# Performance work log

Measured on AMD Instinct MI355X. Metric: run time of the kernel, lower is better.

## Reference

```python
import jax, jax.numpy as jnp
import numpy as np
from jax import lax

# Dimensions (see shape_source)
B, J, I, E, H = 256, 128, 64, 512, 512   # batch, target len, source len, embed, hidden
MAXJW = 128                               # max jump width
WJ = 2 * MAXJW + 1                        # size of jump-width set (257)
ALPHA_P0 = 1.0
EPS = 1e-29


def setup_inputs() -> dict:
    key = jax.random.key(0)
    ks = jax.random.split(key, 10)
    return {
        "y_hidden": jax.random.normal(ks[0], (B, J, E), jnp.float32),
        "y_hidden_null": jax.random.normal(ks[1], (1, 1, E), jnp.float32),
        "W_trans": jax.random.normal(ks[2], (E, H), jnp.float32) * 0.02,
        "b_trans": jnp.zeros((H,), jnp.float32),
        "W_jump": jax.random.normal(ks[3], (H, WJ), jnp.float32) * 0.02,
        "b_jump": jnp.zeros((WJ,), jnp.float32),
        "W_p0": jax.random.normal(ks[4], (H, 1), jnp.float32) * 0.02,
        "b_p0": jnp.zeros((1,), jnp.float32),
        # emission probs p(source_t | target_state_k), kept near 1 to avoid
        # underflow of the unrescaled HMM forward product (as in original).
        "emission": jax.random.uniform(ks[5], (B, 2 * J, I), jnp.float32) * 0.5 + 0.75,
        "source_lengths": jax.random.randint(ks[6], (B,), 1, I + 1, dtype=jnp.int32),
        "target_lengths": jax.random.randint(ks[7], (B,), 1, J + 1, dtype=jnp.int32),
    }


def _build_transition(y_hidden, y_hidden_null, W_trans, b_trans, W_jump, b_jump, W_p0, b_p0):
    # get_transition: Dense(tanh) -> Dense(softmax) jump widths; Dense(sigmoid) p0.
    ts = jnp.tanh(y_hidden @ W_trans + b_trans)           # [B,J,H]
    ts_null = jnp.tanh(y_hidden_null @ W_trans + b_trans) # [1,1,H]
    jump_prob = jax.nn.softmax(ts @ W_jump + b_jump, axis=-1)  # [B,J,WJ]
    p0_scalar = ALPHA_P0 * jax.nn.sigmoid(ts_null @ W_p0 + b_p0)[0, 0, 0]
    p0 = jnp.broadcast_to(p0_scalar, (y_hidden.shape[0], J))  # tile to [B,J]
    # gather jump widths: row i takes jump_prob[:, i, MAXJW + k - i] for k in [0,J)
    idx = MAXJW + jnp.arange(J)[None, :] - jnp.arange(J)[:, None]        # [J,J]
    idxb = jnp.broadcast_to(idx[None], (jump_prob.shape[0], J, J))
    jw = jnp.take_along_axis(jump_prob, idxb, axis=2)                    # [B,J,J]
    jw = jw * (1.0 - p0[:, :, None]) / jnp.sum(jw, axis=2, keepdims=True)
    diag_p0 = p0[:, :, None] * jnp.eye(J, dtype=jw.dtype)                # [B,J,J]
    T_half = jnp.concatenate([jw, diag_p0], axis=2)                      # [B,J,2J]
    return jnp.concatenate([T_half, T_half], axis=1)                     # [B,2J,2J]


def reference(y_hidden, y_hidden_null, W_trans, b_trans, W_jump, b_jump,
              W_p0, b_p0, emission, source_lengths, target_lengths):
    T = _build_transition(y_hidden, y_hidden_null, W_trans, b_trans,
                          W_jump, b_jump, W_p0, b_p0)       # [B,2J,2J]
    e = jnp.transpose(emission, (2, 0, 1))                  # [I,B,2J]
    # tf.scan with no initializer: f_0 = emission at source position 0
    f0 = e[0]

    def step(f, et):
        f_next = jnp.einsum('bj,bjk->bk', f, T) * et        # forward recursion
        return f_next, f_next

    _, fs = lax.scan(step, f0, e[1:])
    fs = jnp.concatenate([f0[None], fs], axis=0)            # [I,B,2J]
    fbt = jnp.transpose(fs, (1, 2, 0))                      # [B,2J,I]
    last_idx = (source_lengths - 1).astype(jnp.int32)[:, None, None]
    last = jnp.take_along_axis(fbt, last_idx, axis=2)[:, :, 0]  # [B,2J]
    m = (jnp.arange(J)[None, :] < target_lengths[:, None]).astype(last.dtype)
    mask = jnp.concatenate([m, m], axis=1)                  # [B,2J]
    return jnp.log(jnp.sum(last * mask, axis=1) + EPS)      # [B]
```

## Files before the change

kernel.cpp:

```cpp
#include <hip/hip_runtime.h>
#include <stdint.h>

typedef __attribute__((ext_vector_type(8))) short bf16x8;
typedef __attribute__((ext_vector_type(4))) float f32x4;

__device__ __forceinline__ unsigned short f2bf(float f) {
  union { float f; unsigned int u; } un; un.f = f;
  unsigned int r = un.u + 0x7fffu + ((un.u >> 16) & 1u);
  return (unsigned short)(r >> 16);
}

__device__ __forceinline__ float bf2f(unsigned short u) {
  union { unsigned int u; float f; } un; un.u = ((unsigned int)u) << 16;
  return un.f;
}

__device__ __forceinline__ float tanh_fast(float x) {
  x = fminf(15.f, fmaxf(-15.f, x));
  float e = __expf(2.f * x);
  return (e - 1.f) / (e + 1.f);
}

__device__ __forceinline__ unsigned int cvt_pk_bf16(float lo, float hi) {
  unsigned int r;
  asm("v_cvt_pk_bf16_f32 %0, %1, %2" : "=v"(r) : "v"(lo), "v"(hi));
  return r;
}

__device__ __forceinline__ void gload_lds16(const void* g, void* l) {
  __builtin_amdgcn_global_load_lds(
      (const __attribute__((address_space(1))) unsigned int*)(unsigned long long)g,
      (__attribute__((address_space(3))) unsigned int*)(unsigned int)(unsigned long long)l,
      16, 0, 0);
}

__global__ __launch_bounds__(256) void cvt_weights(
    const float* __restrict__ Wt_in, const float* __restrict__ Wj_in,
    unsigned short* __restrict__ wt, unsigned short* __restrict__ wj) {
  const int i = blockIdx.x * 256 + threadIdx.x;
  if (i < 512 * 512) {
    const int c = i >> 9, r = i & 511;
    wt[i] = f2bf(Wt_in[(size_t)r * 512 + c]);
  } else {
    const int j = i - 512 * 512;
    const int c = j >> 9, r = j & 511;
    wj[j] = f2bf(Wj_in[(size_t)r * 257 + c]);
  }
}

__global__ __launch_bounds__(512) void p0_kernel(
    const float* __restrict__ ynull, const float* __restrict__ W_trans,
    const float* __restrict__ b_trans, const float* __restrict__ W_p0,
    const float* __restrict__ b_p0, float* __restrict__ p0buf) {
  __shared__ float red[512];
  const int hh = threadIdx.x;
  float acc = 0.f;
  for (int e = 0; e < 512; ++e) acc = fmaf(ynull[e], W_trans[(size_t)e * 512 + hh], acc);
  const float ts = tanhf(acc + b_trans[hh]);
  red[hh] = ts * W_p0[hh];
  __syncthreads();
  for (int s = 256; s > 0; s >>= 1) {
    if (hh < s) red[hh] += red[hh + s];
    __syncthreads();
  }
  if (hh == 0) {
    const float z = red[0] + b_p0[0];
    const float p0 = 1.f / (1.f + __expf(-z));
    p0buf[0] = p0;
    p0buf[1] = 1.f - p0;
  }
}


__global__ __launch_bounds__(256, 2) void gemm_af32(
    const float* __restrict__ A, const unsigned short* __restrict__ Bt,
    const float* __restrict__ bias, unsigned short* __restrict__ Cout,
    int M, int N, int K) {
  __shared__ unsigned short sA[2][128 * 32];
  __shared__ unsigned short sB[2][128 * 32];
  const int tid = threadIdx.x;
  const int lane = tid & 63;
  const int wave = tid >> 6;
  const int wr = wave >> 1, wc = wave & 1;
  const int m0 = blockIdx.x * 128, n0 = blockIdx.y * 128;

  f32x4 acc[4][4] = {};

  const int srow = lane >> 2;
  const int sl = lane & 3;
  const int scol = sl * 8;
  const int wsz = (srow >> 1) & 3;
  const int scolw = (sl ^ wsz) * 8;
  const int c0 = wave * 2, c1 = wave * 2 + 1;
  const float* Af0 = A + (size_t)(m0 + c0 * 16 + srow) * K + scol;
  const float* Af1 = A + (size_t)(m0 + c1 * 16 + srow) * K + scol;
  const unsigned short* Br0 = Bt + (size_t)(n0 + c0 * 16 + srow) * K + scolw;
  const unsigned short* Br1 = Bt + (size_t)(n0 + c1 * 16 + srow) * K + scolw;

  const int r15 = lane & 15;
  const int oslot = ((lane >> 4) ^ ((r15 >> 1) & 3)) * 8;
  const int nt = K >> 5;

  auto writeA = [&](int bi, const float4& v00, const float4& v01,
                    const float4& v10, const float4& v11) {
    union { unsigned int u[4]; bf16x8 v; } p;
    p.u[0] = cvt_pk_bf16(v00.x, v00.y);
    p.u[1] = cvt_pk_bf16(v00.z, v00.w);
    p.u[2] = cvt_pk_bf16(v01.x, v01.y);
    p.u[3] = cvt_pk_bf16(v01.z, v01.w);
    *reinterpret_cast<bf16x8*>(&sA[bi][c0 * 512 + srow * 32 + scolw]) = p.v;
    p.u[0] = cvt_pk_bf16(v10.x, v10.y);
    p.u[1] = cvt_pk_bf16(v10.z, v10.w);
    p.u[2] = cvt_pk_bf16(v11.x, v11.y);
    p.u[3] = cvt_pk_bf16(v11.z, v11.w);
    *reinterpret_cast<bf16x8*>(&sA[bi][c1 * 512 + srow * 32 + scolw]) = p.v;
  };
  auto stageB = [&](int bi, int t) {
    gload_lds16(Br0 + t * 32, &sB[bi][c0 * 512]);
    gload_lds16(Br1 + t * 32, &sB[bi][c1 * 512]);
  };
  auto compute = [&](int bi) {
    bf16x8 af[4], bfr[4];
#pragma unroll
    for (int mi = 0; mi < 4; ++mi)
      af[mi] = *reinterpret_cast<const bf16x8*>(
          &sA[bi][(wr * 64 + mi * 16 + r15) * 32 + oslot]);
#pragma unroll
    for (int ni = 0; ni < 4; ++ni)
      bfr[ni] = *reinterpret_cast<const bf16x8*>(
          &sB[bi][(wc * 64 + ni * 16 + r15) * 32 + oslot]);
#pragma unroll
    for (int mi = 0; mi < 4; ++mi)
#pragma unroll
      for (int ni = 0; ni < 4; ++ni)
        acc[mi][ni] = __builtin_amdgcn_mfma_f32_16x16x32_bf16(
            af[mi], bfr[ni], acc[mi][ni], 0, 0, 0);
  };

  float4 x0 = *reinterpret_cast<const float4*>(Af0);
  float4 x1 = *reinterpret_cast<const float4*>(Af0 + 4);
  float4 x2 = *reinterpret_cast<const float4*>(Af1);
  float4 x3 = *reinterpret_cast<const float4*>(Af1 + 4);
  float4 y0 = *reinterpret_cast<const float4*>(Af0 + 32);
  float4 y1 = *reinterpret_cast<const float4*>(Af0 + 36);
  float4 y2 = *reinterpret_cast<const float4*>(Af1 + 32);
  float4 y3 = *reinterpret_cast<const float4*>(Af1 + 36);
  writeA(0, x0, x1, x2, x3);
  stageB(0, 0);
  __syncthreads();

  for (int t = 0; t < nt; t += 2) {
    if (t + 1 < nt) {
      writeA(1, y0, y1, y2, y3);
      stageB(1, t + 1);
    }
    if (t + 2 < nt) {
      x0 = *reinterpret_cast<const float4*>(Af0 + (t + 2) * 32);
      x1 = *reinterpret_cast<const float4*>(Af0 + (t + 2) * 32 + 4);
      x2 = *reinterpret_cast<const float4*>(Af1 + (t + 2) * 32);
      x3 = *reinterpret_cast<const float4*>(Af1 + (t + 2) * 32 + 4);
    }
    compute(0);
    __syncthreads();
    if (t + 2 < nt) {
      writeA(0, x0, x1, x2, x3);
      stageB(0, t + 2);
    }
    if (t + 3 < nt) {
      y0 = *reinterpret_cast<const float4*>(Af0 + (t + 3) * 32);
      y1 = *reinterpret_cast<const float4*>(Af0 + (t + 3) * 32 + 4);
      y2 = *reinterpret_cast<const float4*>(Af1 + (t + 3) * 32);
      y3 = *reinterpret_cast<const float4*>(Af1 + (t + 3) * 32 + 4);
    }
    if (t + 1 < nt) compute(1);
    __syncthreads();
  }

  const int crow0 = m0 + wr * 64 + (lane >> 4) * 4;
  const int ccol0 = n0 + wc * 64 + r15;
#pragma unroll
  for (int mi = 0; mi < 4; ++mi) {
#pragma unroll
    for (int ni = 0; ni < 4; ++ni) {
      const int gcol = ccol0 + ni * 16;
      const float bv = bias[gcol];
#pragma unroll
      for (int r = 0; r < 4; ++r) {
        const int grow = crow0 + mi * 16 + r;
        Cout[(size_t)grow * N + gcol] = f2bf(tanh_fast(acc[mi][ni][r] + bv));
      }
    }
  }
}

__global__ __launch_bounds__(256, 2) void gemm_tt(
    const unsigned short* __restrict__ A, const unsigned short* __restrict__ Bt,
    const float* __restrict__ bias, unsigned short* __restrict__ Cout,
    int M, int N, int K) {
  __shared__ unsigned short sA[2][128 * 32];
  __shared__ unsigned short sB[2][128 * 32];
  const int tid = threadIdx.x;
  const int lane = tid & 63;
  const int wave = tid >> 6;
  const int wr = wave >> 1, wc = wave & 1;
  const int m0 = blockIdx.x * 128, n0 = blockIdx.y * 128;

  f32x4 acc[4][4] = {};

  const int srow = lane >> 2;
  const int sl = lane & 3;
  const int wsz = (srow >> 1) & 3;
  const int scolw = (sl ^ wsz) * 8;
  const int c0 = wave * 2, c1 = wave * 2 + 1;
  const unsigned short* Ar0 = A + (size_t)(m0 + c0 * 16 + srow) * K + scolw;
  const unsigned short* Ar1 = A + (size_t)(m0 + c1 * 16 + srow) * K + scolw;
  const unsigned short* Br0 = Bt + (size_t)(n0 + c0 * 16 + srow) * K + scolw;
  const unsigned short* Br1 = Bt + (size_t)(n0 + c1 * 16 + srow) * K + scolw;

  const int r15 = lane & 15;
  const int oslot = ((lane >> 4) ^ ((r15 >> 1) & 3)) * 8;
  const int nt = K >> 5;

  auto stage = [&](int bi, int t) {
    gload_lds16(Ar0 + t * 32, &sA[bi][c0 * 512]);
    gload_lds16(Ar1 + t * 32, &sA[bi][c1 * 512]);
    gload_lds16(Br0 + t * 32, &sB[bi][c0 * 512]);
    gload_lds16(Br1 + t * 32, &sB[bi][c1 * 512]);
  };
  auto compute = [&](int bi) {
    bf16x8 af[4], bfr[4];
#pragma unroll
    for (int mi = 0; mi < 4; ++mi)
      af[mi] = *reinterpret_cast<const bf16x8*>(
          &sA[bi][(wr * 64 + mi * 16 + r15) * 32 + oslot]);
#pragma unroll
    for (int ni = 0; ni < 4; ++ni)
      bfr[ni] = *reinterpret_cast<const bf16x8*>(
          &sB[bi][(wc * 64 + ni * 16 + r15) * 32 + oslot]);
#pragma unroll
    for (int mi = 0; mi < 4; ++mi)
#pragma unroll
      for (int ni = 0; ni < 4; ++ni)
        acc[mi][ni] = __builtin_amdgcn_mfma_f32_16x16x32_bf16(
            af[mi], bfr[ni], acc[mi][ni], 0, 0, 0);
  };

  stage(0, 0);
  __syncthreads();
  for (int t = 0; t < nt; t += 2) {
    if (t + 1 < nt) stage(1, t + 1);
    compute(0);
    __syncthreads();
    if (t + 2 < nt) stage(0, t + 2);
    if (t + 1 < nt) compute(1);
    __syncthreads();
  }

  const int crow0 = m0 + wr * 64 + (lane >> 4) * 4;
  const int ccol0 = n0 + wc * 64 + r15;
#pragma unroll
  for (int mi = 0; mi < 4; ++mi) {
#pragma unroll
    for (int ni = 0; ni < 4; ++ni) {
      const int gcol = ccol0 + ni * 16;
      const float bv = bias[gcol];
#pragma unroll
      for (int r = 0; r < 4; ++r) {
        const int grow = crow0 + mi * 16 + r;
        Cout[(size_t)grow * N + gcol] = f2bf(acc[mi][ni][r] + bv);
      }
    }
  }
}

__global__ __launch_bounds__(256) void wsoftmax_kernel(
    const unsigned short* __restrict__ logits, const float* __restrict__ p0buf,
    unsigned short* __restrict__ jwout) {
  const int lane = threadIdx.x & 63;
  const int wave = threadIdx.x >> 6;
  const int row = blockIdx.x * 4 + wave;
  const int i = row & 127;
  const unsigned short* lrow = logits + (size_t)row * 256 + (128 - i);
  const float v0 = bf2f(lrow[lane]);
  const float v1 = bf2f(lrow[lane + 64]);
  float mx = fmaxf(v0, v1);
#pragma unroll
  for (int off = 32; off > 0; off >>= 1) mx = fmaxf(mx, __shfl_xor(mx, off));
  const float e0 = __expf(v0 - mx);
  const float e1 = __expf(v1 - mx);
  float s = e0 + e1;
#pragma unroll
  for (int off = 32; off > 0; off >>= 1) s += __shfl_xor(s, off);
  const float scale = p0buf[1] / s;
  unsigned short* orow = jwout + (size_t)row * 128;
  orow[lane] = f2bf(e0 * scale);
  orow[lane + 64] = f2bf(e1 * scale);
}

#define SE_STRIDE 264
__global__ __launch_bounds__(256, 1) void forward_fused(
    const unsigned short* __restrict__ jwb,
    const float* __restrict__ emission,
    const float* __restrict__ p0buf, const int* __restrict__ slen_p,
    const int* __restrict__ tlen_p, float* __restrict__ out) {
  __shared__ __align__(16) float se[64 * SE_STRIDE];
  __shared__ __align__(16) unsigned short gl16[128];
  const int b = blockIdx.x;
  const int tid = threadIdx.x;
  const float* eb = emission + (size_t)b * 16384;

  bf16x8 bfr[4][8];
  const int l = tid & 63;
  const int m = l & 15;
  const int q = l >> 4;

  if (tid >= 64) {
#pragma unroll
    for (int it = 0; it < 6; ++it) {
      const int tau = (tid - 64) + 192 * it;
      if (tau < 1024) {
        const int t0 = (tau & 15) * 4;
        const int mm = (tau >> 4) & 15;
        const int nt0 = ((tau >> 8) & 1) * 4;
        const int half = (tau >> 9) & 1;
        const int kbase = half * 128 + nt0 * 16 + mm;
        const float4 v0 = *reinterpret_cast<const float4*>(&eb[(size_t)(kbase) * 64 + t0]);
        const float4 v1 = *reinterpret_cast<const float4*>(&eb[(size_t)(kbase + 16) * 64 + t0]);
        const float4 v2 = *reinterpret_cast<const float4*>(&eb[(size_t)(kbase + 32) * 64 + t0]);
        const float4 v3 = *reinterpret_cast<const float4*>(&eb[(size_t)(kbase + 48) * 64 + t0]);
        const int jinv0 = half * 128 + mm * 8 + nt0;
        float* d = &se[(size_t)t0 * SE_STRIDE + jinv0];
        *reinterpret_cast<float4*>(d) = (float4){v0.x, v1.x, v2.x, v3.x};
        *reinterpret_cast<float4*>(d + SE_STRIDE) = (float4){v0.y, v1.y, v2.y, v3.y};
        *reinterpret_cast<float4*>(d + 2 * SE_STRIDE) = (float4){v0.z, v1.z, v2.z, v3.z};
        *reinterpret_cast<float4*>(d + 3 * SE_STRIDE) = (float4){v0.w, v1.w, v2.w, v3.w};
      }
    }
  } else {
    const unsigned short* jwt = jwb + (size_t)b * 16384;
#pragma unroll
    for (int kt = 0; kt < 4; ++kt) {
      const int r0 = kt * 32 + q * 8;
#pragma unroll
      for (int nt = 0; nt < 8; ++nt) {
        const int c = nt * 16 + m;
        bf16x8 v;
#pragma unroll
        for (int j = 0; j < 8; ++j) v[j] = (short)jwt[(size_t)(r0 + j) * 128 + c];
        bfr[kt][nt] = v;
      }
    }
  }
  __syncthreads();
  if (tid >= 64) return;

  const float p0 = p0buf[0];
  const int S = slen_p[b];
  const int T = tlen_p[b];

  float gown[8];
  {
    const float4 i0a = *reinterpret_cast<const float4*>(&se[m * 8]);
    const float4 i0b = *reinterpret_cast<const float4*>(&se[m * 8 + 4]);
    const float4 i1a = *reinterpret_cast<const float4*>(&se[128 + m * 8]);
    const float4 i1b = *reinterpret_cast<const float4*>(&se[128 + m * 8 + 4]);
    gown[0] = i0a.x + i1a.x; gown[1] = i0a.y + i1a.y;
    gown[2] = i0a.z + i1a.z; gown[3] = i0a.w + i1a.w;
    gown[4] = i0b.x + i1b.x; gown[5] = i0b.y + i1b.y;
    gown[6] = i0b.z + i1b.z; gown[7] = i0b.w + i1b.w;
  }
  gl16[(2 * q) * 16 + m]     = f2bf(gown[2 * q]);
  gl16[(2 * q + 1) * 16 + m] = f2bf(gown[2 * q + 1]);

  for (int t = 1; t < S; ++t) {
    const float* st = &se[(size_t)t * SE_STRIDE];
    const float4 pe0a = *reinterpret_cast<const float4*>(&st[m * 8]);
    const float4 pe0b = *reinterpret_cast<const float4*>(&st[m * 8 + 4]);
    const float4 pe1a = *reinterpret_cast<const float4*>(&st[128 + m * 8]);
    const float4 pe1b = *reinterpret_cast<const float4*>(&st[128 + m * 8 + 4]);
    const float e0[8] = {pe0a.x, pe0a.y, pe0a.z, pe0a.w, pe0b.x, pe0b.y, pe0b.z, pe0b.w};
    const float e1[8] = {pe1a.x, pe1a.y, pe1a.z, pe1a.w, pe1b.x, pe1b.y, pe1b.z, pe1b.w};
    float h[8];
#pragma unroll
    for (int nt = 0; nt < 8; ++nt) h[nt] = gown[nt] * (p0 * e1[nt]);
    bf16x8 af[4];
#pragma unroll
    for (int kt = 0; kt < 4; ++kt)
      af[kt] = *reinterpret_cast<const bf16x8*>(&gl16[kt * 32 + q * 8]);
    f32x4 acc[8];
#pragma unroll
    for (int nt = 0; nt < 8; ++nt) {
      f32x4 a = __builtin_amdgcn_mfma_f32_16x16x32_bf16(
          af[0], bfr[0][nt], (f32x4){0.f, 0.f, 0.f, 0.f}, 0, 0, 0);
      a = __builtin_amdgcn_mfma_f32_16x16x32_bf16(af[1], bfr[1][nt], a, 0, 0, 0);
      a = __builtin_amdgcn_mfma_f32_16x16x32_bf16(af[2], bfr[2][nt], a, 0, 0, 0);
      acc[nt] = __builtin_amdgcn_mfma_f32_16x16x32_bf16(af[3], bfr[3][nt], a, 0, 0, 0);
    }
#pragma unroll
    for (int nt = 0; nt < 8; ++nt) gown[nt] = fmaf(acc[nt][0], e0[nt], h[nt]);
    gl16[(2 * q) * 16 + m]     = f2bf(gown[2 * q]);
    gl16[(2 * q + 1) * 16 + m] = f2bf(gown[2 * q + 1]);
  }

  float val = 0.f;
#pragma unroll
  for (int nt = 0; nt < 8; ++nt)
    if (nt * 16 + m < T) val += gown[nt];
#pragma unroll
  for (int off = 1; off < 16; off <<= 1) val += __shfl_xor(val, off);
  if (l == 0) out[b] = logf(val + 1e-29f);
}

extern "C" void kernel_launch(void* const* d_in, const int* in_sizes, int n_in,
                              void* d_out, int out_size, void* d_ws, size_t ws_size,
                              hipStream_t stream) {
  const float* y_hidden = (const float*)d_in[0];
  const float* y_null   = (const float*)d_in[1];
  const float* W_trans  = (const float*)d_in[2];
  const float* b_trans  = (const float*)d_in[3];
  const float* W_jump   = (const float*)d_in[4];
  const float* b_jump   = (const float*)d_in[5];
  const float* W_p0     = (const float*)d_in[6];
  const float* b_p0     = (const float*)d_in[7];
  const float* emission = (const float*)d_in[8];
  const int* slen = (const int*)d_in[9];
  const int* tlen = (const int*)d_in[10];
  float* out = (float*)d_out;

  char* ws = (char*)d_ws;
  unsigned short* ts16  = (unsigned short*)ws;
  unsigned short* lg16  = (unsigned short*)(ws + 33554432);
  unsigned short* wt16t = (unsigned short*)(ws + 50331648);
  unsigned short* wj16t = (unsigned short*)(ws + 50855936);
  float* p0buf          = (float*)(ws + 51118080);
  unsigned short* jwb16 = (unsigned short*)(ws + 51118336);

  cvt_weights<<<dim3(1536), dim3(256), 0, stream>>>(W_trans, W_jump, wt16t, wj16t);
  p0_kernel<<<dim3(1), dim3(512), 0, stream>>>(y_null, W_trans, b_trans, W_p0, b_p0, p0buf);

  gemm_af32<<<dim3(256, 4), dim3(256), 0, stream>>>(y_hidden, wt16t, b_trans, ts16,
                                                    32768, 512, 512);
  gemm_tt<<<dim3(256, 2), dim3(256), 0, stream>>>(ts16, wj16t, b_jump, lg16,
                                                  32768, 256, 512);
  wsoftmax_kernel<<<dim3(8192), dim3(256), 0, stream>>>(lg16, p0buf, jwb16);
  forward_fused<<<dim3(256), dim3(256), 0, stream>>>(jwb16, emission, p0buf,
                                                     slen, tlen, out);
}
```

Measured before the change: 116.2 us.

## Restructure GEMMs to stage B half-panels in LDS and stream A from registers

Both projection GEMMs are rewritten to load a 128x256 half of the B (weight) panel into LDS at a time with an XOR swizzle. Each wave now owns 32 full rows and reads A fragments directly from global memory into registers, converting fp32 to bf16 inline for the first GEMM. This removes the per-32-K double-buffered LDS staging of A and most of the barriers. In exchange there is no overlap between B staging and compute, A loads are issued per-wave without LDS sharing, and LDS use rises to 64KB per block, which may limit occupancy.

```diff
diff --git a/kernel.cpp b/kernel.cpp
--- a/kernel.cpp
+++ b/kernel.cpp
@@ -72,202 +72,130 @@
 }
 
 
-__global__ __launch_bounds__(256, 2) void gemm_af32(
+__device__ __forceinline__ void stage_half(
+    const unsigned short* __restrict__ Bt, unsigned short* sB,
+    int n0, int h, int wave, int lane) {
+  const int ln = lane >> 5;
+  const int slot = lane & 31;
+#pragma unroll
+  for (int c = 0; c < 16; ++c) {
+    const int cw = wave * 16 + c;
+    const int row = 2 * cw + ln;
+    const unsigned short* src =
+        Bt + (size_t)(n0 + row) * 512 + h * 256 + ((slot ^ (row & 7)) * 8);
+    gload_lds16(src, &sB[cw * 512]);
+  }
+}
+
+__global__ __launch_bounds__(256, 2) void gemm1_panel(
     const float* __restrict__ A, const unsigned short* __restrict__ Bt,
-    const float* __restrict__ bias, unsigned short* __restrict__ Cout,
-    int M, int N, int K) {
-  __shared__ unsigned short sA[2][128 * 32];
-  __shared__ unsigned short sB[2][128 * 32];
+    const float* __restrict__ bias, unsigned short* __restrict__ Cout) {
+  __shared__ unsigned short sB[128 * 256];
   const int tid = threadIdx.x;
   const int lane = tid & 63;
   const int wave = tid >> 6;
-  const int wr = wave >> 1, wc = wave & 1;
+  const int r15 = lane & 15;
+  const int q = lane >> 4;
   const int m0 = blockIdx.x * 128, n0 = blockIdx.y * 128;
 
-  f32x4 acc[4][4] = {};
-
-  const int srow = lane >> 2;
-  const int sl = lane & 3;
-  const int scol = sl * 8;
-  const int wsz = (srow >> 1) & 3;
-  const int scolw = (sl ^ wsz) * 8;
-  const int c0 = wave * 2, c1 = wave * 2 + 1;
-  const float* Af0 = A + (size_t)(m0 + c0 * 16 + srow) * K + scol;
-  const float* Af1 = A + (size_t)(m0 + c1 * 16 + srow) * K + scol;
-  const unsigned short* Br0 = Bt + (size_t)(n0 + c0 * 16 + srow) * K + scolw;
-  const unsigned short* Br1 = Bt + (size_t)(n0 + c1 * 16 + srow) * K + scolw;
-
-  const int r15 = lane & 15;
-  const int oslot = ((lane >> 4) ^ ((r15 >> 1) & 3)) * 8;
-  const int nt = K >> 5;
-
-  auto writeA = [&](int bi, const float4& v00, const float4& v01,
-                    const float4& v10, const float4& v11) {
-    union { unsigned int u[4]; bf16x8 v; } p;
-    p.u[0] = cvt_pk_bf16(v00.x, v00.y);
-    p.u[1] = cvt_pk_bf16(v00.z, v00.w);
-    p.u[2] = cvt_pk_bf16(v01.x, v01.y);
-    p.u[3] = cvt_pk_bf16(v01.z, v01.w);
-    *reinterpret_cast<bf16x8*>(&sA[bi][c0 * 512 + srow * 32 + scolw]) = p.v;
-    p.u[0] = cvt_pk_bf16(v10.x, v10.y);
-    p.u[1] = cvt_pk_bf16(v10.z, v10.w);
-    p.u[2] = cvt_pk_bf16(v11.x, v11.y);
-    p.u[3] = cvt_pk_bf16(v11.z, v11.w);
-    *reinterpret_cast<bf16x8*>(&sA[bi][c1 * 512 + srow * 32 + scolw]) = p.v;
-  };
-  auto stageB = [&](int bi, int t) {
-    gload_lds16(Br0 + t * 32, &sB[bi][c0 * 512]);
-    gload_lds16(Br1 + t * 32, &sB[bi][c1 * 512]);
-  };
-  auto compute = [&](int bi) {
-    bf16x8 af[4], bfr[4];
-#pragma unroll
-    for (int mi = 0; mi < 4; ++mi)
-      af[mi] = *reinterpret_cast<const bf16x8*>(
-          &sA[bi][(wr * 64 + mi * 16 + r15) * 32 + oslot]);
-#pragma unroll
-    for (int ni = 0; ni < 4; ++ni)
-      bfr[ni] = *reinterpret_cast<const bf16x8*>(
-          &sB[bi][(wc * 64 + ni * 16 + r15) * 32 + oslot]);
-#pragma unroll
-    for (int mi = 0; mi < 4; ++mi)
-#pragma unroll
-      for (int ni = 0; ni < 4; ++ni)
-        acc[mi][ni] = __builtin_amdgcn_mfma_f32_16x16x32_bf16(
-            af[mi], bfr[ni], acc[mi][ni], 0, 0, 0);
-  };
-
-  float4 x0 = *reinterpret_cast<const float4*>(Af0);
-  float4 x1 = *reinterpret_cast<const float4*>(Af0 + 4);
-  float4 x2 = *reinterpret_cast<const float4*>(Af1);
-  float4 x3 = *reinterpret_cast<const float4*>(Af1 + 4);
-  float4 y0 = *reinterpret_cast<const float4*>(Af0 + 32);
-  float4 y1 = *reinterpret_cast<const float4*>(Af0 + 36);
-  float4 y2 = *reinterpret_cast<const float4*>(Af1 + 32);
-  float4 y3 = *reinterpret_cast<const float4*>(Af1 + 36);
-  writeA(0, x0, x1, x2, x3);
-  stageB(0, 0);
-  __syncthreads();
-
-  for (int t = 0; t < nt; t += 2) {
-    if (t + 1 < nt) {
-      writeA(1, y0, y1, y2, y3);
-      stageB(1, t + 1);
-    }
-    if (t + 2 < nt) {
-      x0 = *reinterpret_cast<const float4*>(Af0 + (t + 2) * 32);
-      x1 = *reinterpret_cast<const float4*>(Af0 + (t + 2) * 32 + 4);
-      x2 = *reinterpret_cast<const float4*>(Af1 + (t + 2) * 32);
-      x3 = *reinterpret_cast<const float4*>(Af1 + (t + 2) * 32 + 4);
-    }
-    compute(0);
-    __syncthreads();
-    if (t + 2 < nt) {
-      writeA(0, x0, x1, x2, x3);
-      stageB(0, t + 2);
-    }
-    if (t + 3 < nt) {
-      y0 = *reinterpret_cast<const float4*>(Af0 + (t + 3) * 32);
-      y1 = *reinterpret_cast<const float4*>(Af0 + (t + 3) * 32 + 4);
-      y2 = *reinterpret_cast<const float4*>(Af1 + (t + 3) * 32);
-      y3 = *reinterpret_cast<const float4*>(Af1 + (t + 3) * 32 + 4);
-    }
-    if (t + 1 < nt) compute(1);
-    __syncthreads();
-  }
-
-  const int crow0 = m0 + wr * 64 + (lane >> 4) * 4;
-  const int ccol0 = n0 + wc * 64 + r15;
-#pragma unroll
-  for (int mi = 0; mi < 4; ++mi) {
-#pragma unroll
-    for (int ni = 0; ni < 4; ++ni) {
-      const int gcol = ccol0 + ni * 16;
+  f32x4 acc[2][8] = {};
+  const float* Arow0 = A + (size_t)(m0 + wave * 32 + r15) * 512;
+  const float* Arow1 = A + (size_t)(m0 + wave * 32 + 16 + r15) * 512;
+  const int sxor = r15 & 7;
+
+  for (int h = 0; h < 2; ++h) {
+    stage_half(Bt, sB, n0, h, wave, lane);
+    __syncthreads();
+#pragma unroll 2
+    for (int kk = 0; kk < 8; ++kk) {
+      const int col = h * 256 + kk * 32 + q * 8;
+      bf16x8 af[2];
+      {
+        const float4 lo0 = *reinterpret_cast<const float4*>(Arow0 + col);
+        const float4 hi0 = *reinterpret_cast<const float4*>(Arow0 + col + 4);
+        const float4 lo1 = *reinterpret_cast<const float4*>(Arow1 + col);
+        const float4 hi1 = *reinterpret_cast<const float4*>(Arow1 + col + 4);
+        union { unsigned int u[4]; bf16x8 v; } p;
+        p.u[0] = cvt_pk_bf16(lo0.x, lo0.y); p.u[1] = cvt_pk_bf16(lo0.z, lo0.w);
+        p.u[2] = cvt_pk_bf16(hi0.x, hi0.y); p.u[3] = cvt_pk_bf16(hi0.z, hi0.w);
+        af[0] = p.v;
+        p.u[0] = cvt_pk_bf16(lo1.x, lo1.y); p.u[1] = cvt_pk_bf16(lo1.z, lo1.w);
+        p.u[2] = cvt_pk_bf16(hi1.x, hi1.y); p.u[3] = cvt_pk_bf16(hi1.z, hi1.w);
+        af[1] = p.v;
+      }
+      const int s0 = kk * 4 + q;
+#pragma unroll
+      for (int ni = 0; ni < 8; ++ni) {
+        const bf16x8 bfr = *reinterpret_cast<const bf16x8*>(
+            &sB[(ni * 16 + r15) * 256 + ((s0 ^ sxor) * 8)]);
+        acc[0][ni] = __builtin_amdgcn_mfma_f32_16x16x32_bf16(af[0], bfr, acc[0][ni], 0, 0, 0);
+        acc[1][ni] = __builtin_amdgcn_mfma_f32_16x16x32_bf16(af[1], bfr, acc[1][ni], 0, 0, 0);
+      }
+    }
+    __syncthreads();
+  }
+
+#pragma unroll
+  for (int mi = 0; mi < 2; ++mi) {
+    const int crow0 = m0 + wave * 32 + mi * 16 + q * 4;
+#pragma unroll
+    for (int ni = 0; ni < 8; ++ni) {
+      const int gcol = n0 + ni * 16 + r15;
       const float bv = bias[gcol];
 #pragma unroll
       for (int r = 0; r < 4; ++r) {
-        const int grow = crow0 + mi * 16 + r;
-        Cout[(size_t)grow * N + gcol] = f2bf(tanh_fast(acc[mi][ni][r] + bv));
-      }
-    }
-  }
-}
-
-__global__ __launch_bounds__(256, 2) void gemm_tt(
+        Cout[(size_t)(crow0 + r) * 512 + gcol] = f2bf(tanh_fast(acc[mi][ni][r] + bv));
+      }
+    }
+  }
+}
+
+__global__ __launch_bounds__(256, 2) void gemm2_panel(
     const unsigned short* __restrict__ A, const unsigned short* __restrict__ Bt,
-    const float* __restrict__ bias, unsigned short* __restrict__ Cout,
-    int M, int N, int K) {
-  __shared__ unsigned short sA[2][128 * 32];
-  __shared__ unsigned short sB[2][128 * 32];
+    const float* __restrict__ bias, unsigned short* __restrict__ Cout) {
+  __shared__ unsigned short sB[128 * 256];
   const int tid = threadIdx.x;
   const int lane = tid & 63;
   const int wave = tid >> 6;
-  const int wr = wave >> 1, wc = wave & 1;
+  const int r15 = lane & 15;
+  const int q = lane >> 4;
   const int m0 = blockIdx.x * 128, n0 = blockIdx.y * 128;
 
-  f32x4 acc[4][4] = {};
-
-  const int srow = lane >> 2;
-  const int sl = lane & 3;
-  const int wsz = (srow >> 1) & 3;
-  const int scolw = (sl ^ wsz) * 8;
-  const int c0 = wave * 2, c1 = wave * 2 + 1;
-  const unsigned short* Ar0 = A + (size_t)(m0 + c0 * 16 + srow) * K + scolw;
-  const unsigned short* Ar1 = A + (size_t)(m0 + c1 * 16 + srow) * K + scolw;
-  const unsigned short* Br0 = Bt + (size_t)(n0 + c0 * 16 + srow) * K + scolw;
-  const unsigned short* Br1 = Bt + (size_t)(n0 + c1 * 16 + srow) * K + scolw;
-
-  const int r15 = lane & 15;
-  const int oslot = ((lane >> 4) ^ ((r15 >> 1) & 3)) * 8;
-  const int nt = K >> 5;
-
-  auto stage = [&](int bi, int t) {
-    gload_lds16(Ar0 + t * 32, &sA[bi][c0 * 512]);
-    gload_lds16(Ar1 + t * 32, &sA[bi][c1 * 512]);
-    gload_lds16(Br0 + t * 32, &sB[bi][c0 * 512]);
-    gload_lds16(Br1 + t * 32, &sB[bi][c1 * 512]);
-  };
-  auto compute = [&](int bi) {
-    bf16x8 af[4], bfr[4];
-#pragma unroll
-    for (int mi = 0; mi < 4; ++mi)
-      af[mi] = *reinterpret_cast<const bf16x8*>(
-          &sA[bi][(wr * 64 + mi * 16 + r15) * 32 + oslot]);
-#pragma unroll
-    for (int ni = 0; ni < 4; ++ni)
-      bfr[ni] = *reinterpret_cast<const bf16x8*>(
-          &sB[bi][(wc * 64 + ni * 16 + r15) * 32 + oslot]);
-#pragma unroll
-    for (int mi = 0; mi < 4; ++mi)
-#pragma unroll
-      for (int ni = 0; ni < 4; ++ni)
-        acc[mi][ni] = __builtin_amdgcn_mfma_f32_16x16x32_bf16(
-            af[mi], bfr[ni], acc[mi][ni], 0, 0, 0);
-  };
-
-  stage(0, 0);
-  __syncthreads();
-  for (int t = 0; t < nt; t += 2) {
-    if (t + 1 < nt) stage(1, t + 1);
-    compute(0);
-    __syncthreads();
-    if (t + 2 < nt) stage(0, t + 2);
-    if (t + 1 < nt) compute(1);
-    __syncthreads();
-  }
-
-  const int crow0 = m0 + wr * 64 + (lane >> 4) * 4;
-  const int ccol0 = n0 + wc * 64 + r15;
-#pragma unroll
-  for (int mi = 0; mi < 4; ++mi) {
-#pragma unroll
-    for (int ni = 0; ni < 4; ++ni) {
-      const int gcol = ccol0 + ni * 16;
+  f32x4 acc[2][8] = {};
+  const unsigned short* Arow0 = A + (size_t)(m0 + wave * 32 + r15) * 512;
+  const unsigned short* Arow1 = A + (size_t)(m0 + wave * 32 + 16 + r15) * 512;
+  const int sxor = r15 & 7;
+
+  for (int h = 0; h < 2; ++h) {
+    stage_half(Bt, sB, n0, h, wave, lane);
+    __syncthreads();
+#pragma unroll 2
+    for (int kk = 0; kk < 8; ++kk) {
+      const int col = h * 256 + kk * 32 + q * 8;
+      const bf16x8 af0 = *reinterpret_cast<const bf16x8*>(Arow0 + col);
+      const bf16x8 af1 = *reinterpret_cast<const bf16x8*>(Arow1 + col);
+      const int s0 = kk * 4 + q;
+#pragma unroll
+      for (int ni = 0; ni < 8; ++ni) {
+        const bf16x8 bfr = *reinterpret_cast<const bf16x8*>(
+            &sB[(ni * 16 + r15) * 256 + ((s0 ^ sxor) * 8)]);
+        acc[0][ni] = __builtin_amdgcn_mfma_f32_16x16x32_bf16(af0, bfr, acc[0][ni], 0, 0, 0);
+        acc[1][ni] = __builtin_amdgcn_mfma_f32_16x16x32_bf16(af1, bfr, acc[1][ni], 0, 0, 0);
+      }
+    }
+    __syncthreads();
+  }
+
+#pragma unroll
+  for (int mi = 0; mi < 2; ++mi) {
+    const int crow0 = m0 + wave * 32 + mi * 16 + q * 4;
+#pragma unroll
+    for (int ni = 0; ni < 8; ++ni) {
+      const int gcol = n0 + ni * 16 + r15;
       const float bv = bias[gcol];
 #pragma unroll
       for (int r = 0; r < 4; ++r) {
-        const int grow = crow0 + mi * 16 + r;
-        Cout[(size_t)grow * N + gcol] = f2bf(acc[mi][ni][r] + bv);
+        Cout[(size_t)(crow0 + r) * 256 + gcol] = f2bf(acc[mi][ni][r] + bv);
       }
     }
   }
@@ -438,10 +366,8 @@
   cvt_weights<<<dim3(1536), dim3(256), 0, stream>>>(W_trans, W_jump, wt16t, wj16t);
   p0_kernel<<<dim3(1), dim3(512), 0, stream>>>(y_null, W_trans, b_trans, W_p0, b_p0, p0buf);
 
-  gemm_af32<<<dim3(256, 4), dim3(256), 0, stream>>>(y_hidden, wt16t, b_trans, ts16,
-                                                    32768, 512, 512);
-  gemm_tt<<<dim3(256, 2), dim3(256), 0, stream>>>(ts16, wj16t, b_jump, lg16,
-                                                  32768, 256, 512);
+  gemm1_panel<<<dim3(256, 4), dim3(256), 0, stream>>>(y_hidden, wt16t, b_trans, ts16);
+  gemm2_panel<<<dim3(256, 2), dim3(256), 0, stream>>>(ts16, wj16t, b_jump, lg16);
   wsoftmax_kernel<<<dim3(8192), dim3(256), 0, stream>>>(lg16, p0buf, jwb16);
   forward_fused<<<dim3(256), dim3(256), 0, stream>>>(jwb16, emission, p0buf,
                                                      slen, tlen, out);
```

New measurement: 130.9 us. 1.13x slower.
